# Kernel optimization log

Measured on AMD Instinct MI355X. Metric: run time of the kernel, lower is better.

Reference implementation:

```python
import jax, jax.numpy as jnp
import numpy as np

N = 100000   # nodes
E = 1600000  # edges
IN = 256
H = 128


def gcn_conv(x, W, b, src, dst, n):
    """PyG GCNConv (eval): self-loops + symmetric normalization + linear + scatter-add."""
    h = x @ W                                   # [n, out]
    loop = jnp.arange(n)
    s = jnp.concatenate([src, loop])            # [E+n]
    d = jnp.concatenate([dst, loop])
    deg = jax.ops.segment_sum(jnp.ones_like(d, dtype=h.dtype), d, num_segments=n)
    dinv = jnp.where(deg > 0, jax.lax.rsqrt(deg), 0.0)
    norm = dinv[s] * dinv[d]                    # [E+n]
    out = jax.ops.segment_sum(h[s] * norm[:, None], d, num_segments=n)
    return out + b


def setup_inputs() -> dict:
    key = jax.random.key(0)
    ks = jax.random.split(key, 8)
    x = jax.random.normal(ks[0], (N, IN), dtype=jnp.float32)
    edge_index = jax.random.randint(ks[1], (2, E), 0, N, dtype=jnp.int64)
    W1 = jax.random.normal(ks[2], (IN, H), dtype=jnp.float32) * (1.0 / np.sqrt(IN))
    b1 = jnp.zeros((H,), dtype=jnp.float32)
    W2 = jax.random.normal(ks[3], (H, H), dtype=jnp.float32) * (1.0 / np.sqrt(H))
    b2 = jnp.zeros((H,), dtype=jnp.float32)
    W3 = jax.random.normal(ks[4], (H, H), dtype=jnp.float32) * (1.0 / np.sqrt(H))
    b3 = jnp.zeros((H,), dtype=jnp.float32)
    return {"x": x, "edge_index": edge_index, "W1": W1, "b1": b1,
            "W2": W2, "b2": b2, "W3": W3, "b3": b3}


def reference(x, edge_index, W1, b1, W2, b2, W3, b3):
    src, dst = edge_index[0], edge_index[1]
    n = x.shape[0]
    h = gcn_conv(x, W1, b1, src, dst, n)
    h = jax.nn.relu(h)                          # dropout inactive in eval
    h = gcn_conv(h, W2, b2, src, dst, n)
    h = jax.nn.relu(h)
    h = gcn_conv(h, W3, b3, src, dst, n)
    return h
```

## Files before the change

### kernel.cpp

```cpp
#include <hip/hip_runtime.h>

#define HDIM 128

typedef unsigned int uint;
typedef unsigned short ushort;
typedef __attribute__((ext_vector_type(8))) short short8;
typedef __attribute__((ext_vector_type(4))) float f32x4;

typedef __attribute__((address_space(3))) uint  lds_u32_t;
typedef const __attribute__((address_space(1))) uint g_u32_t;
#define GLDS16(gp, lp) __builtin_amdgcn_global_load_lds((g_u32_t*)(gp), (lds_u32_t*)(lp), 16, 0, 0)

__device__ inline ushort f2bf(float f) {
    uint u = __float_as_uint(f);
    uint rounding = 0x7fffu + ((u >> 16) & 1u);
    return (ushort)((u + rounding) >> 16);
}
__device__ inline float bf2f(ushort h) { return __uint_as_float(((uint)h) << 16); }


__global__ __launch_bounds__(256) void k_count(const int* __restrict__ dst,
                                               int* __restrict__ cnt,
                                               int* __restrict__ rank, int e) {
    int i = blockIdx.x * 256 + threadIdx.x;
    if (i < e) rank[i] = atomicAdd(&cnt[dst[i]], 1);
}

__global__ __launch_bounds__(256) void k_dinv(const int* __restrict__ cnt,
                                              float* __restrict__ dinv, int n) {
    int i = blockIdx.x * 256 + threadIdx.x;
    if (i < n) dinv[i] = rsqrtf((float)(cnt[i] + 1));
}

__global__ __launch_bounds__(256) void k_scan1(const int* __restrict__ cnt,
                                               int* __restrict__ offs,
                                               int* __restrict__ bsum, int n) {
    __shared__ int sm[256];
    int tid = threadIdx.x;
    int i = blockIdx.x * 256 + tid;
    int v = (i < n) ? cnt[i] : 0;
    sm[tid] = v;
    __syncthreads();
    for (int off = 1; off < 256; off <<= 1) {
        int t = (tid >= off) ? sm[tid - off] : 0;
        __syncthreads();
        sm[tid] += t;
        __syncthreads();
    }
    if (i < n) offs[i] = sm[tid] - v;
    if (tid == 255) bsum[blockIdx.x] = sm[255];
}

__global__ __launch_bounds__(512) void k_scan2(int* __restrict__ bsum, int nb) {
    __shared__ int sm[512];
    int tid = threadIdx.x;
    int v = (tid < nb) ? bsum[tid] : 0;
    sm[tid] = v;
    __syncthreads();
    for (int off = 1; off < 512; off <<= 1) {
        int t = (tid >= off) ? sm[tid - off] : 0;
        __syncthreads();
        sm[tid] += t;
        __syncthreads();
    }
    if (tid < nb) bsum[tid] = sm[tid] - v;
}

__global__ __launch_bounds__(256) void k_scan3(int* __restrict__ offs,
                                               const int* __restrict__ bsum,
                                               int n, int e) {
    int i = blockIdx.x * 256 + threadIdx.x;
    if (i < n) offs[i] += bsum[blockIdx.x];
    if (i == 0) offs[n] = e;
}

__global__ __launch_bounds__(256) void k_fill(const int* __restrict__ src,
                                              const int* __restrict__ dst,
                                              const int* __restrict__ offs,
                                              const int* __restrict__ rank,
                                              int* __restrict__ csr, int e) {
    int i = blockIdx.x * 256 + threadIdx.x;
    if (i < e) {
        csr[offs[dst[i]] + rank[i]] = src[i];
    }
}


__global__ __launch_bounds__(256) void k_prep_w(const float* __restrict__ W,
                                                ushort* __restrict__ wt, int K) {
    int idx = blockIdx.x * 256 + threadIdx.x;
    if (idx < K * HDIM) {
        int k = idx >> 7;
        int c = idx & 127;
        wt[(k >> 5) * 4096 + c * 32 + (k & 31)] = f2bf(W[idx]);
    }
}


template<int NKT>
__global__ __launch_bounds__(512)
void k_mm(const ushort* __restrict__ XP,
          const ushort* __restrict__ WP,
          const float* __restrict__ dinv,
          ushort* __restrict__ g, int n)
{
    __shared__ ushort w[NKT * 4096];

    const int tid  = threadIdx.x;
    const int wv   = tid >> 6;
    const int lane = tid & 63;
    const int r    = lane & 15;
    const int gq   = lane >> 4;

    #pragma unroll
    for (int i = 0; i < NKT; i++) {
        int off = (i * 512 + tid) * 8;
        GLDS16(WP + off, w + off);
    }

    const int tile   = blockIdx.x * 8 + wv;
    const int ntiles = (n + 15) / 16;
    const bool twork = tile < ntiles;
    int rowr = twork ? tile * 16 + r : 0;
    const bool rok = twork && (rowr < n);
    if (twork && rowr >= n) rowr = n - 1;

    const size_t n32 = (size_t)n * 32;

    short8 xc[NKT];
    if (twork) {
        const size_t ro = (size_t)rowr * 32 + gq * 8;
        #pragma unroll
        for (int kt = 0; kt < NKT; kt++)
            xc[kt] = *(const short8*)(XP + kt * n32 + ro);
    }

    __syncthreads();

    if (!twork) return;

    f32x4 acc[8];
    #pragma unroll
    for (int m = 0; m < 8; m++) acc[m] = (f32x4){0.f, 0.f, 0.f, 0.f};

    #pragma unroll
    for (int kt = 0; kt < NKT; kt++) {
        #pragma unroll
        for (int m = 0; m < 8; m++) {
            short8 wf = *(const short8*)&w[kt * 4096 + (m * 16 + r) * 32 + gq * 8];
            acc[m] = __builtin_amdgcn_mfma_f32_16x16x32_bf16(wf, xc[kt], acc[m], 0, 0, 0);
        }
    }

    if (rok) {
        float di = dinv[rowr];
        #pragma unroll
        for (int m = 0; m < 8; m++) {
            f32x4 a = acc[m];
            uint2 pk;
            pk.x = (uint)f2bf(a[0] * di) | ((uint)f2bf(a[1] * di) << 16);
            pk.y = (uint)f2bf(a[2] * di) | ((uint)f2bf(a[3] * di) << 16);
            *(uint2*)(g + (size_t)rowr * HDIM + m * 16 + gq * 4) = pk;
        }
    }
}


__global__ __launch_bounds__(512)
void k_mm_f32(const float* __restrict__ X,
              const ushort* __restrict__ WP,
              const float* __restrict__ dinv,
              ushort* __restrict__ g, int n)
{
    __shared__ ushort w[8 * 4096];

    const int tid  = threadIdx.x;
    const int wv   = tid >> 6;
    const int lane = tid & 63;
    const int r    = lane & 15;
    const int gq   = lane >> 4;

    #pragma unroll
    for (int i = 0; i < 8; i++) {
        int off = (i * 512 + tid) * 8;
        GLDS16(WP + off, w + off);
    }

    const int tile   = blockIdx.x * 8 + wv;
    const int ntiles = (n + 15) / 16;
    const bool twork = tile < ntiles;
    int rowr = twork ? tile * 16 + r : 0;
    const bool rok = twork && (rowr < n);
    if (twork && rowr >= n) rowr = n - 1;

    f32x4 xf[16];
    if (twork) {
        const f32x4* xp = (const f32x4*)(X + (size_t)rowr * 256);
        #pragma unroll
        for (int kt = 0; kt < 8; kt++) {
            xf[kt * 2]     = xp[kt * 8 + gq * 2];
            xf[kt * 2 + 1] = xp[kt * 8 + gq * 2 + 1];
        }
    }

    __syncthreads();

    if (!twork) return;

    f32x4 acc[8];
    #pragma unroll
    for (int m = 0; m < 8; m++) acc[m] = (f32x4){0.f, 0.f, 0.f, 0.f};

    #pragma unroll
    for (int kt = 0; kt < 8; kt++) {
        float v[8] = {xf[kt*2][0], xf[kt*2][1], xf[kt*2][2], xf[kt*2][3],
                      xf[kt*2+1][0], xf[kt*2+1][1], xf[kt*2+1][2], xf[kt*2+1][3]};
        short8 bh;
        #pragma unroll
        for (int q = 0; q < 8; q++) bh[q] = (short)f2bf(v[q]);
        #pragma unroll
        for (int m = 0; m < 8; m++) {
            short8 wf = *(const short8*)&w[kt * 4096 + (m * 16 + r) * 32 + gq * 8];
            acc[m] = __builtin_amdgcn_mfma_f32_16x16x32_bf16(wf, bh, acc[m], 0, 0, 0);
        }
    }

    if (rok) {
        float di = dinv[rowr];
        #pragma unroll
        for (int m = 0; m < 8; m++) {
            f32x4 a = acc[m];
            uint2 pk;
            pk.x = (uint)f2bf(a[0] * di) | ((uint)f2bf(a[1] * di) << 16);
            pk.y = (uint)f2bf(a[2] * di) | ((uint)f2bf(a[3] * di) << 16);
            *(uint2*)(g + (size_t)rowr * HDIM + m * 16 + gq * 4) = pk;
        }
    }
}


template<bool RELU, bool EMIT_PLANE>
__global__ __launch_bounds__(256) void k_gather(const ushort* __restrict__ g,
                                                const int* __restrict__ csr,
                                                const int* __restrict__ offs,
                                                const float* __restrict__ dinv,
                                                const float* __restrict__ bias,
                                                float* __restrict__ out,
                                                ushort* __restrict__ ap, int n)
{
    int t    = blockIdx.x * 256 + threadIdx.x;
    int node = t >> 4;
    int l    = t & 15;
    if (node >= n) return;

    int e0 = offs[node];
    int e1 = offs[node + 1];

    float a0 = 0.f, a1 = 0.f, a2 = 0.f, a3 = 0.f,
          a4 = 0.f, a5 = 0.f, a6 = 0.f, a7 = 0.f;

    auto ACC = [&](uint4 u) {
        a0 += bf2f((ushort)(u.x & 0xffff)); a1 += bf2f((ushort)(u.x >> 16));
        a2 += bf2f((ushort)(u.y & 0xffff)); a3 += bf2f((ushort)(u.y >> 16));
        a4 += bf2f((ushort)(u.z & 0xffff)); a5 += bf2f((ushort)(u.z >> 16));
        a6 += bf2f((ushort)(u.w & 0xffff)); a7 += bf2f((ushort)(u.w >> 16));
    };

    ACC(*(const uint4*)(g + (size_t)node * HDIM + l * 8));

    int e = e0;
    for (; e + 4 <= e1; e += 4) {
        int s0 = csr[e], s1 = csr[e + 1], s2 = csr[e + 2], s3 = csr[e + 3];
        uint4 v0 = *(const uint4*)(g + (size_t)s0 * HDIM + l * 8);
        uint4 v1 = *(const uint4*)(g + (size_t)s1 * HDIM + l * 8);
        uint4 v2 = *(const uint4*)(g + (size_t)s2 * HDIM + l * 8);
        uint4 v3 = *(const uint4*)(g + (size_t)s3 * HDIM + l * 8);
        ACC(v0); ACC(v1); ACC(v2); ACC(v3);
    }
    for (; e < e1; e++) {
        int s = csr[e];
        ACC(*(const uint4*)(g + (size_t)s * HDIM + l * 8));
    }

    float di = dinv[node];
    float4 b0 = *(const float4*)(bias + l * 8);
    float4 b1 = *(const float4*)(bias + l * 8 + 4);
    float o0 = fmaf(di, a0, b0.x), o1 = fmaf(di, a1, b0.y);
    float o2 = fmaf(di, a2, b0.z), o3 = fmaf(di, a3, b0.w);
    float o4 = fmaf(di, a4, b1.x), o5 = fmaf(di, a5, b1.y);
    float o6 = fmaf(di, a6, b1.z), o7 = fmaf(di, a7, b1.w);
    if (RELU) {
        o0 = fmaxf(o0, 0.f); o1 = fmaxf(o1, 0.f); o2 = fmaxf(o2, 0.f); o3 = fmaxf(o3, 0.f);
        o4 = fmaxf(o4, 0.f); o5 = fmaxf(o5, 0.f); o6 = fmaxf(o6, 0.f); o7 = fmaxf(o7, 0.f);
    }
    if (EMIT_PLANE) {
        uint4 ph;
        ph.x = (uint)f2bf(o0) | ((uint)f2bf(o1) << 16);
        ph.y = (uint)f2bf(o2) | ((uint)f2bf(o3) << 16);
        ph.z = (uint)f2bf(o4) | ((uint)f2bf(o5) << 16);
        ph.w = (uint)f2bf(o6) | ((uint)f2bf(o7) << 16);
        size_t base = (size_t)(l >> 2) * ((size_t)n * 32) + (size_t)node * 32 + (l & 3) * 8;
        *(uint4*)(ap + base) = ph;
    } else {
        float4 w0 = make_float4(o0, o1, o2, o3);
        float4 w1 = make_float4(o4, o5, o6, o7);
        *(float4*)(out + (size_t)node * HDIM + l * 8)     = w0;
        *(float4*)(out + (size_t)node * HDIM + l * 8 + 4) = w1;
    }
}


extern "C" void kernel_launch(void* const* d_in, const int* in_sizes, int n_in,
                              void* d_out, int out_size, void* d_ws, size_t ws_size,
                              hipStream_t stream)
{
    const float* x  = (const float*)d_in[0];
    const int*   ei = (const int*)d_in[1];
    const float* W1 = (const float*)d_in[2];
    const float* b1 = (const float*)d_in[3];
    const float* W2 = (const float*)d_in[4];
    const float* b2 = (const float*)d_in[5];
    const float* W3 = (const float*)d_in[6];
    const float* b3 = (const float*)d_in[7];
    float* out = (float*)d_out;

    const int n = in_sizes[0] / 256;
    const int E = in_sizes[1] / 2;
    const int* src = ei;
    const int* dst = ei + E;

    char*   ws   = (char*)d_ws;
    float*  dinv = (float*)(ws);
    int*    cnt  = (int*)(ws + (512 << 10));
    int*    offs = (int*)(ws + (1 << 20));
    int*    bsum = (int*)(ws + 1536 * 1024);
    int*    csr  = (int*)(ws + 1600 * 1024);
    int*    rank = (int*)(ws + (size_t)(8 << 20));
    ushort* wt   = (ushort*)(ws + 14848 * 1024);
    ushort* g    = (ushort*)(ws + (size_t)(16 << 20));
    ushort* xp   = (ushort*)(ws + (size_t)(42 << 20));

    dim3 blk(256);
    int ngrid = (n + 255) / 256;
    int egrid = (E + 255) / 256;

    hipMemsetAsync(cnt, 0, (size_t)n * 4, stream);
    k_count<<<egrid, blk, 0, stream>>>(dst, cnt, rank, E);
    k_dinv<<<ngrid, blk, 0, stream>>>(cnt, dinv, n);
    k_scan1<<<ngrid, blk, 0, stream>>>(cnt, offs, bsum, n);
    k_scan2<<<1, 512, 0, stream>>>(bsum, ngrid);
    k_scan3<<<ngrid, blk, 0, stream>>>(offs, bsum, n, E);
    k_fill<<<egrid, blk, 0, stream>>>(src, dst, offs, rank, csr, E);

    int ntiles   = (n + 15) / 16;
    int mm_grid  = (ntiles + 7) / 8;
    int gat_grid = (int)(((size_t)n * 16 + 255) / 256);

    k_prep_w<<<(256 * HDIM + 255) / 256, blk, 0, stream>>>(W1, wt, 256);
    k_mm_f32<<<mm_grid, 512, 0, stream>>>(x, wt, dinv, g, n);
    k_gather<true, true><<<gat_grid, blk, 0, stream>>>(g, csr, offs, dinv, b1, nullptr, xp, n);
    k_prep_w<<<(128 * HDIM + 255) / 256, blk, 0, stream>>>(W2, wt, 128);
    k_mm<4><<<mm_grid, 512, 0, stream>>>(xp, wt, dinv, g, n);
    k_gather<true, true><<<gat_grid, blk, 0, stream>>>(g, csr, offs, dinv, b2, nullptr, xp, n);
    k_prep_w<<<(128 * HDIM + 255) / 256, blk, 0, stream>>>(W3, wt, 128);
    k_mm<4><<<mm_grid, 512, 0, stream>>>(xp, wt, dinv, g, n);
    k_gather<false, false><<<gat_grid, blk, 0, stream>>>(g, csr, offs, dinv, b3, out, nullptr, n);
}
```

Measured before the change: 359.6 us.

## Fuse neighbor aggregation with next-layer matmul through LDS staging

Adds a k_gmm kernel for layers 2 and 3. Each wave aggregates its 16-node tile (including the self loop, applying bias and ReLU), writes the bf16 result into shared memory, and immediately runs the MFMA matmul against the next layer's weights. This drops the round-trip of the intermediate plane buffer through global memory and removes two kernel launches. In exchange each wave now processes its 16 rows' gathers serially, and the block needs more LDS, which may reduce occupancy and latency hiding for the irregular gathers.

After: 377.1 us. 4.9% more time.

```diff
diff --git a/kernel.cpp b/kernel.cpp
--- a/kernel.cpp
+++ b/kernel.cpp
@@ -97,75 +97,6 @@
 }
 
 
-template<int NKT>
-__global__ __launch_bounds__(512)
-void k_mm(const ushort* __restrict__ XP,
-          const ushort* __restrict__ WP,
-          const float* __restrict__ dinv,
-          ushort* __restrict__ g, int n)
-{
-    __shared__ ushort w[NKT * 4096];
-
-    const int tid  = threadIdx.x;
-    const int wv   = tid >> 6;
-    const int lane = tid & 63;
-    const int r    = lane & 15;
-    const int gq   = lane >> 4;
-
-    #pragma unroll
-    for (int i = 0; i < NKT; i++) {
-        int off = (i * 512 + tid) * 8;
-        GLDS16(WP + off, w + off);
-    }
-
-    const int tile   = blockIdx.x * 8 + wv;
-    const int ntiles = (n + 15) / 16;
-    const bool twork = tile < ntiles;
-    int rowr = twork ? tile * 16 + r : 0;
-    const bool rok = twork && (rowr < n);
-    if (twork && rowr >= n) rowr = n - 1;
-
-    const size_t n32 = (size_t)n * 32;
-
-    short8 xc[NKT];
-    if (twork) {
-        const size_t ro = (size_t)rowr * 32 + gq * 8;
-        #pragma unroll
-        for (int kt = 0; kt < NKT; kt++)
-            xc[kt] = *(const short8*)(XP + kt * n32 + ro);
-    }
-
-    __syncthreads();
-
-    if (!twork) return;
-
-    f32x4 acc[8];
-    #pragma unroll
-    for (int m = 0; m < 8; m++) acc[m] = (f32x4){0.f, 0.f, 0.f, 0.f};
-
-    #pragma unroll
-    for (int kt = 0; kt < NKT; kt++) {
-        #pragma unroll
-        for (int m = 0; m < 8; m++) {
-            short8 wf = *(const short8*)&w[kt * 4096 + (m * 16 + r) * 32 + gq * 8];
-            acc[m] = __builtin_amdgcn_mfma_f32_16x16x32_bf16(wf, xc[kt], acc[m], 0, 0, 0);
-        }
-    }
-
-    if (rok) {
-        float di = dinv[rowr];
-        #pragma unroll
-        for (int m = 0; m < 8; m++) {
-            f32x4 a = acc[m];
-            uint2 pk;
-            pk.x = (uint)f2bf(a[0] * di) | ((uint)f2bf(a[1] * di) << 16);
-            pk.y = (uint)f2bf(a[2] * di) | ((uint)f2bf(a[3] * di) << 16);
-            *(uint2*)(g + (size_t)rowr * HDIM + m * 16 + gq * 4) = pk;
-        }
-    }
-}
-
-
 __global__ __launch_bounds__(512)
 void k_mm_f32(const float* __restrict__ X,
               const ushort* __restrict__ WP,
@@ -239,14 +170,127 @@
 }
 
 
-template<bool RELU, bool EMIT_PLANE>
-__global__ __launch_bounds__(256) void k_gather(const ushort* __restrict__ g,
-                                                const int* __restrict__ csr,
-                                                const int* __restrict__ offs,
-                                                const float* __restrict__ dinv,
-                                                const float* __restrict__ bias,
-                                                float* __restrict__ out,
-                                                ushort* __restrict__ ap, int n)
+__global__ __launch_bounds__(512)
+void k_gmm(const ushort* __restrict__ g_in,
+           const int* __restrict__ csr,
+           const int* __restrict__ offs,
+           const float* __restrict__ dinv,
+           const float* __restrict__ bias,
+           const ushort* __restrict__ WP,
+           ushort* __restrict__ g_out, int n)
+{
+    __shared__ ushort w[4 * 4096];
+    __shared__ ushort xb[8][16][128];
+
+    const int tid  = threadIdx.x;
+    const int wv   = tid >> 6;
+    const int lane = tid & 63;
+
+    #pragma unroll
+    for (int i = 0; i < 4; i++) {
+        int off = (i * 512 + tid) * 8;
+        GLDS16(WP + off, w + off);
+    }
+
+    const int tile   = blockIdx.x * 8 + wv;
+    const int ntiles = (n + 15) / 16;
+    const bool twork = tile < ntiles;
+
+    const int c16 = lane & 15;
+    const int g4  = lane >> 4;
+    if (twork) {
+        #pragma unroll
+        for (int s = 0; s < 4; s++) {
+            int row  = s * 4 + g4;
+            int node = tile * 16 + row;
+            float a0 = 0.f, a1 = 0.f, a2 = 0.f, a3 = 0.f,
+                  a4 = 0.f, a5 = 0.f, a6 = 0.f, a7 = 0.f;
+            if (node < n) {
+                auto ACC = [&](uint4 u) {
+                    a0 += bf2f((ushort)(u.x & 0xffff)); a1 += bf2f((ushort)(u.x >> 16));
+                    a2 += bf2f((ushort)(u.y & 0xffff)); a3 += bf2f((ushort)(u.y >> 16));
+                    a4 += bf2f((ushort)(u.z & 0xffff)); a5 += bf2f((ushort)(u.z >> 16));
+                    a6 += bf2f((ushort)(u.w & 0xffff)); a7 += bf2f((ushort)(u.w >> 16));
+                };
+                int e0 = offs[node];
+                int e1 = offs[node + 1];
+                ACC(*(const uint4*)(g_in + (size_t)node * HDIM + c16 * 8));
+                int e = e0;
+                for (; e + 4 <= e1; e += 4) {
+                    int s0 = csr[e], s1 = csr[e + 1], s2 = csr[e + 2], s3 = csr[e + 3];
+                    uint4 v0 = *(const uint4*)(g_in + (size_t)s0 * HDIM + c16 * 8);
+                    uint4 v1 = *(const uint4*)(g_in + (size_t)s1 * HDIM + c16 * 8);
+                    uint4 v2 = *(const uint4*)(g_in + (size_t)s2 * HDIM + c16 * 8);
+                    uint4 v3 = *(const uint4*)(g_in + (size_t)s3 * HDIM + c16 * 8);
+                    ACC(v0); ACC(v1); ACC(v2); ACC(v3);
+                }
+                for (; e < e1; e++) {
+                    int ss = csr[e];
+                    ACC(*(const uint4*)(g_in + (size_t)ss * HDIM + c16 * 8));
+                }
+                float di = dinv[node];
+                float4 b0 = *(const float4*)(bias + c16 * 8);
+                float4 b1 = *(const float4*)(bias + c16 * 8 + 4);
+                a0 = fmaxf(fmaf(di, a0, b0.x), 0.f); a1 = fmaxf(fmaf(di, a1, b0.y), 0.f);
+                a2 = fmaxf(fmaf(di, a2, b0.z), 0.f); a3 = fmaxf(fmaf(di, a3, b0.w), 0.f);
+                a4 = fmaxf(fmaf(di, a4, b1.x), 0.f); a5 = fmaxf(fmaf(di, a5, b1.y), 0.f);
+                a6 = fmaxf(fmaf(di, a6, b1.z), 0.f); a7 = fmaxf(fmaf(di, a7, b1.w), 0.f);
+            }
+            uint4 ph;
+            ph.x = (uint)f2bf(a0) | ((uint)f2bf(a1) << 16);
+            ph.y = (uint)f2bf(a2) | ((uint)f2bf(a3) << 16);
+            ph.z = (uint)f2bf(a4) | ((uint)f2bf(a5) << 16);
+            ph.w = (uint)f2bf(a6) | ((uint)f2bf(a7) << 16);
+            *(uint4*)&xb[wv][c16][row * 8] = ph;
+        }
+    }
+
+    __syncthreads();
+
+    if (!twork) return;
+
+    const int r  = lane & 15;
+    const int gq = lane >> 4;
+
+    short8 xc[4];
+    #pragma unroll
+    for (int kt = 0; kt < 4; kt++)
+        xc[kt] = *(const short8*)&xb[wv][kt * 4 + gq][r * 8];
+
+    f32x4 acc[8];
+    #pragma unroll
+    for (int m = 0; m < 8; m++) acc[m] = (f32x4){0.f, 0.f, 0.f, 0.f};
+
+    #pragma unroll
+    for (int kt = 0; kt < 4; kt++) {
+        #pragma unroll
+        for (int m = 0; m < 8; m++) {
+            short8 wf = *(const short8*)&w[kt * 4096 + (m * 16 + r) * 32 + gq * 8];
+            acc[m] = __builtin_amdgcn_mfma_f32_16x16x32_bf16(wf, xc[kt], acc[m], 0, 0, 0);
+        }
+    }
+
+    int rowr = tile * 16 + r;
+    if (rowr < n) {
+        float di = dinv[rowr];
+        #pragma unroll
+        for (int m = 0; m < 8; m++) {
+            f32x4 a = acc[m];
+            uint2 pk;
+            pk.x = (uint)f2bf(a[0] * di) | ((uint)f2bf(a[1] * di) << 16);
+            pk.y = (uint)f2bf(a[2] * di) | ((uint)f2bf(a[3] * di) << 16);
+            *(uint2*)(g_out + (size_t)rowr * HDIM + m * 16 + gq * 4) = pk;
+        }
+    }
+}
+
+
+__global__ __launch_bounds__(256) void k_gather_out(const ushort* __restrict__ g,
+                                                    const int* __restrict__ csr,
+                                                    const int* __restrict__ offs,
+                                                    const float* __restrict__ dinv,
+                                                    const float* __restrict__ bias,
+                                                    float* __restrict__ out, int n)
 {
     int t    = blockIdx.x * 256 + threadIdx.x;
     int node = t >> 4;
@@ -285,28 +329,12 @@
     float di = dinv[node];
     float4 b0 = *(const float4*)(bias + l * 8);
     float4 b1 = *(const float4*)(bias + l * 8 + 4);
-    float o0 = fmaf(di, a0, b0.x), o1 = fmaf(di, a1, b0.y);
-    float o2 = fmaf(di, a2, b0.z), o3 = fmaf(di, a3, b0.w);
-    float o4 = fmaf(di, a4, b1.x), o5 = fmaf(di, a5, b1.y);
-    float o6 = fmaf(di, a6, b1.z), o7 = fmaf(di, a7, b1.w);
-    if (RELU) {
-        o0 = fmaxf(o0, 0.f); o1 = fmaxf(o1, 0.f); o2 = fmaxf(o2, 0.f); o3 = fmaxf(o3, 0.f);
-        o4 = fmaxf(o4, 0.f); o5 = fmaxf(o5, 0.f); o6 = fmaxf(o6, 0.f); o7 = fmaxf(o7, 0.f);
-    }
-    if (EMIT_PLANE) {
-        uint4 ph;
-        ph.x = (uint)f2bf(o0) | ((uint)f2bf(o1) << 16);
-        ph.y = (uint)f2bf(o2) | ((uint)f2bf(o3) << 16);
-        ph.z = (uint)f2bf(o4) | ((uint)f2bf(o5) << 16);
-        ph.w = (uint)f2bf(o6) | ((uint)f2bf(o7) << 16);
-        size_t base = (size_t)(l >> 2) * ((size_t)n * 32) + (size_t)node * 32 + (l & 3) * 8;
-        *(uint4*)(ap + base) = ph;
-    } else {
-        float4 w0 = make_float4(o0, o1, o2, o3);
-        float4 w1 = make_float4(o4, o5, o6, o7);
-        *(float4*)(out + (size_t)node * HDIM + l * 8)     = w0;
-        *(float4*)(out + (size_t)node * HDIM + l * 8 + 4) = w1;
-    }
+    float4 w0 = make_float4(fmaf(di, a0, b0.x), fmaf(di, a1, b0.y),
+                            fmaf(di, a2, b0.z), fmaf(di, a3, b0.w));
+    float4 w1 = make_float4(fmaf(di, a4, b1.x), fmaf(di, a5, b1.y),
+                            fmaf(di, a6, b1.z), fmaf(di, a7, b1.w));
+    *(float4*)(out + (size_t)node * HDIM + l * 8)     = w0;
+    *(float4*)(out + (size_t)node * HDIM + l * 8 + 4) = w1;
 }
 
 
@@ -337,8 +365,9 @@
     int*    csr  = (int*)(ws + 1600 * 1024);
     int*    rank = (int*)(ws + (size_t)(8 << 20));
     ushort* wt   = (ushort*)(ws + 14848 * 1024);
-    ushort* g    = (ushort*)(ws + (size_t)(16 << 20));
-    ushort* xp   = (ushort*)(ws + (size_t)(42 << 20));
+    ushort* g1   = (ushort*)(ws + (size_t)(16 << 20));
+    ushort* g2   = (ushort*)(ws + (size_t)(42 << 20));
+    ushort* g3   = (ushort*)(ws + (size_t)(68 << 20));
 
     dim3 blk(256);
     int ngrid = (n + 255) / 256;
@@ -357,12 +386,10 @@
     int gat_grid = (int)(((size_t)n * 16 + 255) / 256);
 
     k_prep_w<<<(256 * HDIM + 255) / 256, blk, 0, stream>>>(W1, wt, 256);
-    k_mm_f32<<<mm_grid, 512, 0, stream>>>(x, wt, dinv, g, n);
-    k_gather<true, true><<<gat_grid, blk, 0, stream>>>(g, csr, offs, dinv, b1, nullptr, xp, n);
+    k_mm_f32<<<mm_grid, 512, 0, stream>>>(x, wt, dinv, g1, n);
     k_prep_w<<<(128 * HDIM + 255) / 256, blk, 0, stream>>>(W2, wt, 128);
-    k_mm<4><<<mm_grid, 512, 0, stream>>>(xp, wt, dinv, g, n);
-    k_gather<true, true><<<gat_grid, blk, 0, stream>>>(g, csr, offs, dinv, b2, nullptr, xp, n);
+    k_gmm<<<mm_grid, 512, 0, stream>>>(g1, csr, offs, dinv, b1, wt, g2, n);
     k_prep_w<<<(128 * HDIM + 255) / 256, blk, 0, stream>>>(W3, wt, 128);
-    k_mm<4><<<mm_grid, 512, 0, stream>>>(xp, wt, dinv, g, n);
-    k_gather<false, false><<<gat_grid, blk, 0, stream>>>(g, csr, offs, dinv, b3, out, nullptr, n);
-}
+    k_gmm<<<mm_grid, 512, 0, stream>>>(g2, csr, offs, dinv, b2, wt, g3, n);
+    k_gather_out<<<gat_grid, blk, 0, stream>>>(g3, csr, offs, dinv, b3, out, n);
+}
```
